# Kernel optimization log

Hardware: AMD Instinct MI355X
Metric: run time of the kernel (lower is better)

The kernel has to match this reference:

```python
import jax, jax.numpy as jnp
import numpy as np

B, M = 128, 1024
D_Z, D_PHI = 1024, 512
H1, H2 = 512, 512


def setup_inputs() -> dict:
    key = jax.random.key(0)
    ks = jax.random.split(key, 8)
    s1 = 1.0 / np.sqrt(D_Z + D_PHI)
    s2 = 1.0 / np.sqrt(H1)
    s3 = 1.0 / np.sqrt(H2)
    return {
        "g_q": jax.random.normal(ks[0], (B, D_Z), jnp.float32),
        "Phi": jax.random.normal(ks[1], (M, D_PHI), jnp.float32),
        "W1": jax.random.normal(ks[2], (D_Z + D_PHI, H1), jnp.float32) * s1,
        "b1": jnp.zeros((H1,), jnp.float32),
        "W2": jax.random.normal(ks[3], (H1, H2), jnp.float32) * s2,
        "b2": jnp.zeros((H2,), jnp.float32),
        "W3": jax.random.normal(ks[4], (H2, 1), jnp.float32) * s3,
        "b3": jnp.zeros((1,), jnp.float32),
    }


def reference(g_q, Phi, W1, b1, W2, b2, W3, b3):
    # net(cat([z_exp, phi_exp])) == (g_q @ W1[:d_z]) broadcast-summed with
    # (Phi @ W1[d_z:]) -- identical math, avoids materializing [B, M, d_z+d_phi].
    d_z = g_q.shape[1]
    hz = g_q @ W1[:d_z]          # [B, H1]
    hp = Phi @ W1[d_z:]          # [M, H1]
    h = hz[:, None, :] + hp[None, :, :] + b1      # [B, M, H1]
    h = jax.nn.gelu(h, approximate=False)         # torch GELU is exact erf form
    h = jax.nn.gelu(h @ W2 + b2, approximate=False)  # [B, M, H2]
    u = h @ W3 + b3                                # [B, M, 1]
    return u[..., 0]                               # [B, M]
```

## Files before the change

kernel.cpp:

```cpp
#include <hip/hip_runtime.h>
#include <hip/hip_bf16.h>


typedef __bf16 bf16x8 __attribute__((ext_vector_type(8)));
typedef float  f32x4  __attribute__((ext_vector_type(4)));
typedef float  f32x2  __attribute__((ext_vector_type(2)));

__device__ __forceinline__ f32x2 gelu_pk(f32x2 x) {
    f32x2 t = x * x;
    f32x2 p = __builtin_elementwise_fma(t, f32x2{0.1029436f, 0.1029436f},
                                        f32x2{2.3022082f, 2.3022082f});
    f32x2 a = p * x;
    f32x2 e;
    e.x = __builtin_amdgcn_exp2f(a.x);
    e.y = __builtin_amdgcn_exp2f(a.y);
    f32x2 d = e + f32x2{1.f, 1.f};
    f32x2 r;
    r.x = __builtin_amdgcn_rcpf(d.x);
    r.y = __builtin_amdgcn_rcpf(d.y);
    return __builtin_elementwise_fma(-x, r, x);
}

__device__ __forceinline__ unsigned int pack_bf16x2(float a, float b) {
    __hip_bfloat162 h = __float22bfloat162_rn(make_float2(a, b));
    return *reinterpret_cast<unsigned int*>(&h);
}
__device__ __forceinline__ float bf_lo(unsigned int u) {
    return __builtin_bit_cast(float, u << 16);
}
__device__ __forceinline__ float bf_hi(unsigned int u) {
    return __builtin_bit_cast(float, u & 0xffff0000u);
}

__global__ __launch_bounds__(256) void wcast_kernel(
    const float* __restrict__ W1, unsigned short* __restrict__ W1F)
{
    __shared__ float tr[64 * 68];
    const int t = threadIdx.x;
    const int id = blockIdx.x;
    const int kt = id >> 3, nt = id & 7;
    const int k0 = kt * 64, n0 = nt * 64;

    {
        int r = t >> 2, c16 = (t & 3) * 16;
        #pragma unroll
        for (int q = 0; q < 4; ++q)
            *(float4*)&tr[r * 68 + c16 + q * 4] =
                *(const float4*)&W1[(k0 + r) * 512 + n0 + c16 + q * 4];
    }
    __syncthreads();
    const int nl = t >> 2, kc16 = (t & 3) * 16;
    unsigned int pk[8];
    #pragma unroll
    for (int i = 0; i < 8; ++i) {
        float f0 = tr[(kc16 + 2 * i    ) * 68 + nl];
        float f1 = tr[(kc16 + 2 * i + 1) * 68 + nl];
        pk[i] = pack_bf16x2(f0, f1);
    }
    const int n  = n0 + nl;
    const int nf = n >> 4;
    #pragma unroll
    for (int h = 0; h < 2; ++h) {
        int kbase = k0 + kc16 + h * 8;
        int kc = kbase >> 5;
        int k8 = (kbase >> 3) & 3;
        int lane = (n & 15) + 16 * k8;
        uint4 v = h ? make_uint4(pk[4], pk[5], pk[6], pk[7])
                    : make_uint4(pk[0], pk[1], pk[2], pk[3]);
        *(uint4*)&W1F[(unsigned)((kc * 32 + nf) * 512 + lane * 8)] = v;
    }
}

__global__ __launch_bounds__(256) void l1w2_kernel(
    const float* __restrict__ g_q, const float* __restrict__ Phi,
    const float* __restrict__ W2,
    const unsigned short* __restrict__ W1F, const float* __restrict__ b1,
    float* __restrict__ hzb, unsigned short* __restrict__ hpb,
    unsigned short* __restrict__ W2F)
{
    __shared__ __align__(16) float trf[64 * 68];
    const int t = threadIdx.x;
    const int id = blockIdx.x;

    if (id < 64) {
        const int kt = id >> 3, nt = id & 7;
        const int k0 = kt * 64, n0 = nt * 64;
        {
            int r = t >> 2, c16 = (t & 3) * 16;
            #pragma unroll
            for (int q = 0; q < 4; ++q)
                *(float4*)&trf[r * 68 + c16 + q * 4] =
                    *(const float4*)&W2[(k0 + r) * 512 + n0 + c16 + q * 4];
        }
        __syncthreads();
        const int nl = t >> 2, kc16 = (t & 3) * 16;
        unsigned int pk[8];
        #pragma unroll
        for (int i = 0; i < 8; ++i) {
            float f0 = trf[(kc16 + 2 * i    ) * 68 + nl];
            float f1 = trf[(kc16 + 2 * i + 1) * 68 + nl];
            pk[i] = pack_bf16x2(f0, f1);
        }
        const int n  = n0 + nl;
        const int nf = n >> 4;
        #pragma unroll
        for (int h = 0; h < 2; ++h) {
            int kbase = k0 + kc16 + h * 8;
            int kc = kbase >> 5;
            int k8 = (kbase >> 3) & 3;
            int lane = (n & 15) + 16 * k8;
            uint4 v = h ? make_uint4(pk[4], pk[5], pk[6], pk[7])
                        : make_uint4(pk[0], pk[1], pk[2], pk[3]);
            *(uint4*)&W2F[(unsigned)((kc * 32 + nf) * 512 + lane * 8)] = v;
        }
    } else {
        unsigned short* lA = (unsigned short*)trf;
        const int bi = id - 64;
        const bool is_hz = bi < 4;
        int rt, ct;
        if (is_hz) { rt = bi >> 1;        ct = bi & 1; }
        else       { rt = (bi - 4) >> 1;  ct = (bi - 4) & 1; }
        const int r0 = rt * 64, c0 = ct * 256;
        const int ld = is_hz ? 1024 : 512;
        const int nkt = is_hz ? 16 : 8;
        const int kcb = is_hz ? 0 : 32;
        const float* src = is_hz ? g_q : Phi;

        const int w = t >> 6;
        const int l = t & 63;

        f32x4 acc[4][4];
        #pragma unroll
        for (int a = 0; a < 4; ++a)
            #pragma unroll
            for (int bf = 0; bf < 4; ++bf)
                acc[a][bf] = f32x4{0.f, 0.f, 0.f, 0.f};

        #pragma unroll 1
        for (int kt = 0; kt < nkt; ++kt) {
            uint4 breg[2][4];
            #pragma unroll
            for (int kk = 0; kk < 2; ++kk)
                #pragma unroll
                for (int bf = 0; bf < 4; ++bf)
                    breg[kk][bf] = *(const uint4*)
                        &W1F[(unsigned)(((kcb + kt * 2 + kk) * 32 +
                                         ct * 16 + w * 4 + bf) * 512 + l * 8)];

            #pragma unroll
            for (int h = 0; h < 2; ++h) {
                int ci = h * 256 + t;
                int arow = ci >> 3, ac = ci & 7;
                const float* srow = src + (unsigned)(r0 + arow) * ld;
                float4 p0 = *(const float4*)&srow[kt * 64 + ac * 8];
                float4 p1 = *(const float4*)&srow[kt * 64 + ac * 8 + 4];
                uint4 pk;
                pk.x = pack_bf16x2(p0.x, p0.y);
                pk.y = pack_bf16x2(p0.z, p0.w);
                pk.z = pack_bf16x2(p1.x, p1.y);
                pk.w = pack_bf16x2(p1.z, p1.w);
                *(uint4*)((char*)lA +
                          (unsigned)(arow * 128 + ((ac ^ (arow & 7)) << 4))) = pk;
            }
            __syncthreads();

            #pragma unroll
            for (int kk = 0; kk < 2; ++kk) {
                const int cch = kk * 4 + (l >> 4);
                bf16x8 af[4];
                #pragma unroll
                for (int a = 0; a < 4; ++a) {
                    int row = 16 * a + (l & 15);
                    unsigned off = (unsigned)(row * 128 + ((cch ^ (row & 7)) << 4));
                    af[a] = __builtin_bit_cast(bf16x8,
                                *(const uint4*)((const char*)lA + off));
                }
                #pragma unroll
                for (int bf = 0; bf < 4; ++bf) {
                    bf16x8 bfr = __builtin_bit_cast(bf16x8, breg[kk][bf]);
                    #pragma unroll
                    for (int a = 0; a < 4; ++a)
                        acc[a][bf] = __builtin_amdgcn_mfma_f32_16x16x32_bf16(
                            af[a], bfr, acc[a][bf], 0, 0, 0);
                }
            }
            __syncthreads();
        }

        const int cl = l & 15, rq = (l >> 4) * 4;
        #pragma unroll
        for (int bf = 0; bf < 4; ++bf) {
            int n = c0 + w * 64 + 16 * bf + cl;
            if (is_hz) {
                float bb = b1[n];
                #pragma unroll
                for (int a = 0; a < 4; ++a)
                    #pragma unroll
                    for (int r = 0; r < 4; ++r)
                        hzb[(unsigned)(r0 + 16 * a + rq + r) * 512 + n] =
                            acc[a][bf][r] + bb;
            } else {
                #pragma unroll
                for (int a = 0; a < 4; ++a)
                    #pragma unroll
                    for (int r = 0; r < 4; ++r) {
                        __hip_bfloat16 v = __float2bfloat16(acc[a][bf][r]);
                        hpb[(unsigned)(r0 + 16 * a + rq + r) * 512 + n] =
                            *reinterpret_cast<unsigned short*>(&v);
                    }
            }
        }
    }
}

__global__ __launch_bounds__(512, 2) void fused_kernel(
    const float* __restrict__ hzb, const unsigned short* __restrict__ hpb,
    const unsigned short* __restrict__ W2F,
    const float* __restrict__ b2, const float* __restrict__ W3,
    const float* __restrict__ b3, float* __restrict__ out)
{
    __shared__ __align__(16) unsigned short lA[2 * 64 * 64];
    __shared__ __align__(16) unsigned short hstage[2 * 64 * 64];
    __shared__ __align__(16) float lhz[512];
    __shared__ float lred[8][64];

    const int t = threadIdx.x;
    const int w = __builtin_amdgcn_readfirstlane(t >> 6);
    const int l = t & 63;
    const int r0 = blockIdx.x * 64;
    const int b  = r0 >> 10;
    const int m0 = r0 & 1023;

    f32x4 acc[4][4];
    #pragma unroll
    for (int a = 0; a < 4; ++a)
        #pragma unroll
        for (int bf = 0; bf < 4; ++bf)
            acc[a][bf] = f32x4{0.f, 0.f, 0.f, 0.f};

    const int arow = t >> 3;
    const int ac   = t & 7;
    const unsigned short* hprow = hpb + (unsigned)(m0 + arow) * 512;
    const float4* lhz4 = (const float4*)lhz;
    const unsigned int awoff = (unsigned)(arow * 128 + ((ac ^ (arow & 7)) << 4));
    const unsigned int hoff  = (unsigned)(t * 16);

    auto HPSTAGE = [&](int kt, int buf) {
        __builtin_amdgcn_global_load_lds(
            (const __attribute__((address_space(1))) void*)(hprow + kt * 64 + ac * 8),
            (__attribute__((address_space(3))) void*)((char*)hstage + buf * 8192 + hoff),
            16, 0, 0);
    };

    auto AGEN = [&](int kt, int abuf) {
        uint4 hv = *(const uint4*)((const char*)hstage + (kt & 1) * 8192 + hoff);
        const int kb = kt * 64 + ac * 8;
        float4 z0 = lhz4[kb >> 2];
        float4 z1 = lhz4[(kb >> 2) + 1];
        f32x2 g0 = gelu_pk(f32x2{bf_lo(hv.x), bf_hi(hv.x)} + f32x2{z0.x, z0.y});
        f32x2 g1 = gelu_pk(f32x2{bf_lo(hv.y), bf_hi(hv.y)} + f32x2{z0.z, z0.w});
        f32x2 g2 = gelu_pk(f32x2{bf_lo(hv.z), bf_hi(hv.z)} + f32x2{z1.x, z1.y});
        f32x2 g3 = gelu_pk(f32x2{bf_lo(hv.w), bf_hi(hv.w)} + f32x2{z1.z, z1.w});
        uint4 pk;
        pk.x = pack_bf16x2(g0.x, g0.y);
        pk.y = pack_bf16x2(g1.x, g1.y);
        pk.z = pack_bf16x2(g2.x, g2.y);
        pk.w = pack_bf16x2(g3.x, g3.y);
        *(uint4*)((char*)lA + (unsigned)(abuf * 8192) + awoff) = pk;
    };

    HPSTAGE(0, 0);
    HPSTAGE(1, 1);
    lhz[t] = hzb[b * 512 + t];
    __syncthreads();
    AGEN(0, 0);
    __syncthreads();

    #pragma unroll 2
    for (int kt = 0; kt < 8; ++kt) {
        if (kt < 6) HPSTAGE(kt + 2, kt & 1);

        uint4 breg[2][4];
        #pragma unroll
        for (int kk = 0; kk < 2; ++kk)
            #pragma unroll
            for (int bf = 0; bf < 4; ++bf)
                breg[kk][bf] = *(const uint4*)
                    &W2F[(unsigned)(((kt * 2 + kk) * 32 + w * 4 + bf) * 512 + l * 8)];

        if (kt < 7) AGEN(kt + 1, (kt + 1) & 1);

        const char* abase = (const char*)lA + (kt & 1) * 8192;
        #pragma unroll
        for (int kk = 0; kk < 2; ++kk) {
            const int cch = kk * 4 + (l >> 4);
            bf16x8 af[4];
            #pragma unroll
            for (int a = 0; a < 4; ++a) {
                int row = 16 * a + (l & 15);
                unsigned off = (unsigned)(row * 128 + ((cch ^ (row & 7)) << 4));
                af[a] = __builtin_bit_cast(bf16x8, *(const uint4*)(abase + off));
            }
            #pragma unroll
            for (int bf = 0; bf < 4; ++bf) {
                bf16x8 bfr = __builtin_bit_cast(bf16x8, breg[kk][bf]);
                #pragma unroll
                for (int a = 0; a < 4; ++a)
                    acc[a][bf] = __builtin_amdgcn_mfma_f32_16x16x32_bf16(
                        af[a], bfr, acc[a][bf], 0, 0, 0);
            }
        }

        __syncthreads();
    }

    float b2v[4], w3v[4];
    #pragma unroll
    for (int bf = 0; bf < 4; ++bf) {
        int n = w * 64 + 16 * bf + (l & 15);
        b2v[bf] = b2[n];
        w3v[bf] = W3[n];
    }
    f32x2 ps[4][2];
    #pragma unroll
    for (int a = 0; a < 4; ++a) {
        ps[a][0] = f32x2{0.f, 0.f};
        ps[a][1] = f32x2{0.f, 0.f};
    }

    #pragma unroll
    for (int bf = 0; bf < 4; ++bf) {
        const f32x2 b2p = {b2v[bf], b2v[bf]};
        const f32x2 w3p = {w3v[bf], w3v[bf]};
        #pragma unroll
        for (int a = 0; a < 4; ++a) {
            f32x2 xlo = f32x2{acc[a][bf][0], acc[a][bf][1]} + b2p;
            f32x2 xhi = f32x2{acc[a][bf][2], acc[a][bf][3]} + b2p;
            ps[a][0] = __builtin_elementwise_fma(gelu_pk(xlo), w3p, ps[a][0]);
            ps[a][1] = __builtin_elementwise_fma(gelu_pk(xhi), w3p, ps[a][1]);
        }
    }

    float psum[4][4];
    #pragma unroll
    for (int a = 0; a < 4; ++a) {
        psum[a][0] = ps[a][0].x; psum[a][1] = ps[a][0].y;
        psum[a][2] = ps[a][1].x; psum[a][3] = ps[a][1].y;
    }

    #pragma unroll
    for (int a = 0; a < 4; ++a)
        #pragma unroll
        for (int r = 0; r < 4; ++r) {
            float v = psum[a][r];
            v += __shfl_xor(v, 1);
            v += __shfl_xor(v, 2);
            v += __shfl_xor(v, 4);
            v += __shfl_xor(v, 8);
            psum[a][r] = v;
        }

    if ((l & 15) == 0) {
        int gb = (l >> 4) * 4;
        #pragma unroll
        for (int a = 0; a < 4; ++a)
            #pragma unroll
            for (int r = 0; r < 4; ++r)
                lred[w][16 * a + gb + r] = psum[a][r];
    }
    __syncthreads();
    if (t < 64) {
        float s = b3[0];
        #pragma unroll
        for (int ww = 0; ww < 8; ++ww) s += lred[ww][t];
        out[r0 + t] = s;
    }
}

extern "C" void kernel_launch(void* const* d_in, const int* in_sizes, int n_in,
                              void* d_out, int out_size, void* d_ws, size_t ws_size,
                              hipStream_t stream) {
    (void)in_sizes; (void)n_in; (void)out_size; (void)ws_size;
    const float* g_q = (const float*)d_in[0];
    const float* Phi = (const float*)d_in[1];
    const float* W1  = (const float*)d_in[2];
    const float* b1  = (const float*)d_in[3];
    const float* W2  = (const float*)d_in[4];
    const float* b2  = (const float*)d_in[5];
    const float* W3  = (const float*)d_in[6];
    const float* b3  = (const float*)d_in[7];
    float* out = (float*)d_out;

    char* ws = (char*)d_ws;
    float*          hzb = (float*)ws;
    unsigned short* hpb = (unsigned short*)(ws + 262144);
    unsigned short* W2F = (unsigned short*)(ws + 1310720);
    unsigned short* W1F = (unsigned short*)(ws + 1835008);

    hipLaunchKernelGGL(wcast_kernel, dim3(192), dim3(256), 0, stream,
                       W1, W1F);
    hipLaunchKernelGGL(l1w2_kernel, dim3(100), dim3(256), 0, stream,
                       g_q, Phi, W2, W1F, b1, hzb, hpb, W2F);
    hipLaunchKernelGGL(fused_kernel, dim3(2048), dim3(512), 0, stream,
                       hzb, hpb, W2F, b2, W3, b3, out);
}
```

Before: 113.5 us.

## Split layer-1 hz GEMM along K into partial sums and widen blocks to 512 threads

```diff
diff --git a/kernel.cpp b/kernel.cpp
--- a/kernel.cpp
+++ b/kernel.cpp
@@ -71,11 +71,11 @@
     }
 }
 
-__global__ __launch_bounds__(256) void l1w2_kernel(
+__global__ __launch_bounds__(512) void l1w2_kernel(
     const float* __restrict__ g_q, const float* __restrict__ Phi,
     const float* __restrict__ W2,
-    const unsigned short* __restrict__ W1F, const float* __restrict__ b1,
-    float* __restrict__ hzb, unsigned short* __restrict__ hpb,
+    const unsigned short* __restrict__ W1F,
+    float* __restrict__ hz_part, unsigned short* __restrict__ hpb,
     unsigned short* __restrict__ W2F)
 {
     __shared__ __align__(16) float trf[64 * 68];
@@ -86,44 +86,39 @@
         const int kt = id >> 3, nt = id & 7;
         const int k0 = kt * 64, n0 = nt * 64;
         {
-            int r = t >> 2, c16 = (t & 3) * 16;
-            #pragma unroll
-            for (int q = 0; q < 4; ++q)
-                *(float4*)&trf[r * 68 + c16 + q * 4] =
-                    *(const float4*)&W2[(k0 + r) * 512 + n0 + c16 + q * 4];
+            int row = t >> 3, col = (t & 7) * 8;
+            *(float4*)&trf[row * 68 + col] =
+                *(const float4*)&W2[(k0 + row) * 512 + n0 + col];
+            *(float4*)&trf[row * 68 + col + 4] =
+                *(const float4*)&W2[(k0 + row) * 512 + n0 + col + 4];
         }
         __syncthreads();
-        const int nl = t >> 2, kc16 = (t & 3) * 16;
-        unsigned int pk[8];
-        #pragma unroll
-        for (int i = 0; i < 8; ++i) {
+        const int nl = t >> 3, kc16 = (t & 7) * 8;
+        unsigned int pk[4];
+        #pragma unroll
+        for (int i = 0; i < 4; ++i) {
             float f0 = trf[(kc16 + 2 * i    ) * 68 + nl];
             float f1 = trf[(kc16 + 2 * i + 1) * 68 + nl];
             pk[i] = pack_bf16x2(f0, f1);
         }
-        const int n  = n0 + nl;
-        const int nf = n >> 4;
-        #pragma unroll
-        for (int h = 0; h < 2; ++h) {
-            int kbase = k0 + kc16 + h * 8;
-            int kc = kbase >> 5;
-            int k8 = (kbase >> 3) & 3;
-            int lane = (n & 15) + 16 * k8;
-            uint4 v = h ? make_uint4(pk[4], pk[5], pk[6], pk[7])
-                        : make_uint4(pk[0], pk[1], pk[2], pk[3]);
-            *(uint4*)&W2F[(unsigned)((kc * 32 + nf) * 512 + lane * 8)] = v;
-        }
+        const int n   = n0 + nl;
+        const int nf  = n >> 4;
+        const int kbase = k0 + kc16;
+        const int kc  = kbase >> 5;
+        const int k8  = (kbase >> 3) & 3;
+        const int lane = (n & 15) + 16 * k8;
+        *(uint4*)&W2F[(unsigned)((kc * 32 + nf) * 512 + lane * 8)] =
+            make_uint4(pk[0], pk[1], pk[2], pk[3]);
     } else {
         unsigned short* lA = (unsigned short*)trf;
         const int bi = id - 64;
         const bool is_hz = bi < 4;
-        int rt, ct;
-        if (is_hz) { rt = bi >> 1;        ct = bi & 1; }
-        else       { rt = (bi - 4) >> 1;  ct = (bi - 4) & 1; }
-        const int r0 = rt * 64, c0 = ct * 256;
+        const int rt = is_hz ? (bi >> 1) : (bi - 4);
+        const int ks = is_hz ? (bi & 1) : 0;
+        const int r0 = rt * 64;
         const int ld = is_hz ? 1024 : 512;
-        const int nkt = is_hz ? 16 : 8;
-        const int kcb = is_hz ? 0 : 32;
+        const int kcb = is_hz ? ks * 16 : 32;
+        const int ksoff = is_hz ? ks * 512 : 0;
         const float* src = is_hz ? g_q : Phi;
 
         const int w = t >> 6;
@@ -136,22 +131,22 @@
             for (int bf = 0; bf < 4; ++bf)
                 acc[a][bf] = f32x4{0.f, 0.f, 0.f, 0.f};
 
+        const int arow = t >> 3;
+        const int ac   = t & 7;
+        const float* srow = src + (unsigned)(r0 + arow) * ld + ksoff;
+        const unsigned int awoff = (unsigned)(arow * 128 + ((ac ^ (arow & 7)) << 4));
+
         #pragma unroll 1
-        for (int kt = 0; kt < nkt; ++kt) {
+        for (int kt = 0; kt < 8; ++kt) {
             uint4 breg[2][4];
             #pragma unroll
             for (int kk = 0; kk < 2; ++kk)
                 #pragma unroll
                 for (int bf = 0; bf < 4; ++bf)
                     breg[kk][bf] = *(const uint4*)
-                        &W1F[(unsigned)(((kcb + kt * 2 + kk) * 32 +
-                                         ct * 16 + w * 4 + bf) * 512 + l * 8)];
-
-            #pragma unroll
-            for (int h = 0; h < 2; ++h) {
-                int ci = h * 256 + t;
-                int arow = ci >> 3, ac = ci & 7;
-                const float* srow = src + (unsigned)(r0 + arow) * ld;
+                        &W1F[(unsigned)(((kcb + kt * 2 + kk) * 32 + w * 4 + bf) * 512 + l * 8)];
+
+            {
                 float4 p0 = *(const float4*)&srow[kt * 64 + ac * 8];
                 float4 p1 = *(const float4*)&srow[kt * 64 + ac * 8 + 4];
                 uint4 pk;
@@ -159,8 +154,7 @@
                 pk.y = pack_bf16x2(p0.z, p0.w);
                 pk.z = pack_bf16x2(p1.x, p1.y);
                 pk.w = pack_bf16x2(p1.z, p1.w);
-                *(uint4*)((char*)lA +
-                          (unsigned)(arow * 128 + ((ac ^ (arow & 7)) << 4))) = pk;
+                *(uint4*)((char*)lA + awoff) = pk;
             }
             __syncthreads();
 
@@ -190,15 +184,14 @@
         const int cl = l & 15, rq = (l >> 4) * 4;
         #pragma unroll
         for (int bf = 0; bf < 4; ++bf) {
-            int n = c0 + w * 64 + 16 * bf + cl;
+            int n = w * 64 + 16 * bf + cl;
             if (is_hz) {
-                float bb = b1[n];
+                float* dst = hz_part + ks * 65536;
                 #pragma unroll
                 for (int a = 0; a < 4; ++a)
                     #pragma unroll
                     for (int r = 0; r < 4; ++r)
-                        hzb[(unsigned)(r0 + 16 * a + rq + r) * 512 + n] =
-                            acc[a][bf][r] + bb;
+                        dst[(unsigned)(r0 + 16 * a + rq + r) * 512 + n] = acc[a][bf][r];
             } else {
                 #pragma unroll
                 for (int a = 0; a < 4; ++a)
@@ -214,7 +207,8 @@
 }
 
 __global__ __launch_bounds__(512, 2) void fused_kernel(
-    const float* __restrict__ hzb, const unsigned short* __restrict__ hpb,
+    const float* __restrict__ hz_part, const float* __restrict__ b1,
+    const unsigned short* __restrict__ hpb,
     const unsigned short* __restrict__ W2F,
     const float* __restrict__ b2, const float* __restrict__ W3,
     const float* __restrict__ b3, float* __restrict__ out)
@@ -271,7 +265,7 @@
 
     HPSTAGE(0, 0);
     HPSTAGE(1, 1);
-    lhz[t] = hzb[b * 512 + t];
+    lhz[t] = hz_part[b * 512 + t] + hz_part[65536 + b * 512 + t] + b1[t];
     __syncthreads();
     AGEN(0, 0);
     __syncthreads();
@@ -392,15 +386,15 @@
     float* out = (float*)d_out;
 
     char* ws = (char*)d_ws;
-    float*          hzb = (float*)ws;
-    unsigned short* hpb = (unsigned short*)(ws + 262144);
-    unsigned short* W2F = (unsigned short*)(ws + 1310720);
-    unsigned short* W1F = (unsigned short*)(ws + 1835008);
+    float*          hz_part = (float*)ws;
+    unsigned short* hpb     = (unsigned short*)(ws + 524288);
+    unsigned short* W2F     = (unsigned short*)(ws + 1572864);
+    unsigned short* W1F     = (unsigned short*)(ws + 2097152);
 
     hipLaunchKernelGGL(wcast_kernel, dim3(192), dim3(256), 0, stream,
                        W1, W1F);
-    hipLaunchKernelGGL(l1w2_kernel, dim3(100), dim3(256), 0, stream,
-                       g_q, Phi, W2, W1F, b1, hzb, hpb, W2F);
+    hipLaunchKernelGGL(l1w2_kernel, dim3(84), dim3(512), 0, stream,
+                       g_q, Phi, W2, W1F, hz_part, hpb, W2F);
     hipLaunchKernelGGL(fused_kernel, dim3(2048), dim3(512), 0, stream,
-                       hzb, hpb, W2F, b2, W3, b3, out);
-}
+                       hz_part, b1, hpb, W2F, b2, W3, b3, out);
+}
```

Measured after the change: 106.5 us, median of 2. -6.2%, faster.
